# Optimization experiments

Hardware: AMD Instinct MI355X
Metric: run time of the kernel (lower is better)

## Reference

```python
import math
import jax, jax.numpy as jnp
import numpy as np

SR = 48000
FRAME_HOP = 240
F0_MIN = 20.0
F0_MAX = 5000.0
F0_BINS = 64
VEL_DIM = 8
N_HARM = 128
NOISE_FFT = 1024
N_NOISE = NOISE_FFT // 2 + 1
HOP = NOISE_FFT // 4
PAD = NOISE_FFT // 2


def lin_interp(x, size):
    # matches F.interpolate(mode='linear', align_corners=False) along last axis
    T_in = x.shape[-1]
    pos = (jnp.arange(size, dtype=jnp.float32) + 0.5) * (T_in / size) - 0.5
    pos = jnp.clip(pos, 0.0, T_in - 1.0)
    lo = jnp.floor(pos).astype(jnp.int32)
    hi = jnp.minimum(lo + 1, T_in - 1)
    fr = pos - lo.astype(jnp.float32)
    return x[..., lo] * (1.0 - fr) + x[..., hi] * fr


def encode_f0(f0):
    f0s = jnp.clip(f0, F0_MIN, None)
    fn = jnp.clip((jnp.log(f0s) - math.log(F0_MIN)) / (math.log(F0_MAX) - math.log(F0_MIN)), 0.0, 1.0)
    i = jnp.arange(1, F0_BINS // 2 + 1, dtype=jnp.float32)
    ang = math.pi * i * fn[..., None]  # (B,T,bins/2)
    enc = jnp.stack([jnp.sin(ang), jnp.cos(ang)], axis=-1).reshape(f0.shape + (F0_BINS,))
    return enc * (f0 > 0).astype(jnp.float32)[..., None]


def encode_velocity(vel):
    vn = jnp.clip(vel.astype(jnp.float32) / 7.0, 0.0, 1.0)
    i = jnp.arange(1, VEL_DIM // 2 + 1, dtype=jnp.float32)
    ang = math.pi * i * vn[..., None]
    return jnp.stack([jnp.sin(ang), jnp.cos(ang)], axis=-1).reshape(vel.shape + (VEL_DIM,))


def gru(x, W_ih, W_hh, b_ih, b_hh):
    # torch nn.GRU, 1 layer, batch_first; gate order r,z,n
    B, T, _ = x.shape
    H = W_hh.shape[1]
    gi = x @ W_ih.T + b_ih  # (B,T,3H)

    def step(h, g):
        gh = h @ W_hh.T + b_hh
        ir, iz, in_ = jnp.split(g, 3, axis=-1)
        hr, hz, hn = jnp.split(gh, 3, axis=-1)
        r = jax.nn.sigmoid(ir + hr)
        z = jax.nn.sigmoid(iz + hz)
        n = jnp.tanh(in_ + r * hn)
        h = (1.0 - z) * n + z * h
        return h, h

    _, hs = jax.lax.scan(step, jnp.zeros((B, H), x.dtype), jnp.swapaxes(gi, 0, 1))
    return jnp.swapaxes(hs, 0, 1)


def harmonic_synth(harm_amps, f0_hz, n_samples, inh):
    # harm_amps (B,T,N), f0_hz (B,T), inh (B,) -> (B,S)
    B, T, N = harm_amps.shape
    a = lin_interp(jnp.transpose(harm_amps, (0, 2, 1)), n_samples)        # (B,N,S)
    f0_up = lin_interp(f0_hz[:, None, :], n_samples)[:, 0]               # (B,S)
    k = jnp.arange(1, N + 1, dtype=jnp.float32)
    stretch = jnp.sqrt(1.0 + inh[:, None] * k ** 2)                      # (B,N)
    inst_freq = f0_up[:, None, :] * (k[None, :] * stretch)[:, :, None]   # (B,N,S)
    mask = (inst_freq < SR * 0.45).astype(a.dtype)
    f0_mean = f0_up.mean(axis=-1)
    n_active = jnp.maximum((k[None, :] * f0_mean[:, None] < SR * 0.45).sum(axis=1), 1).astype(a.dtype)
    phase = jnp.cumsum(2.0 * jnp.pi * inst_freq / SR, axis=-1)
    sig = (a * mask * jnp.sin(phase)).sum(axis=1)
    return sig / n_active[:, None]


def noise_synth(noise_mags, f0_hz, n_samples, noise):
    # noise_mags (B,T,513), noise (B,S) -> (B,S)
    B, T, N = noise_mags.shape
    window = 0.5 - 0.5 * jnp.cos(2.0 * jnp.pi * jnp.arange(NOISE_FFT, dtype=jnp.float32) / NOISE_FFT)  # hann, periodic
    padded = jnp.pad(noise, ((0, 0), (PAD, PAD)), mode='reflect')
    T_stft = 1 + n_samples // HOP
    idx = jnp.arange(T_stft)[:, None] * HOP + jnp.arange(NOISE_FFT)[None, :]  # (T_stft, n_fft)
    frames = padded[:, idx] * window                                          # (B,T_stft,n_fft)
    spec = jnp.fft.rfft(frames)                                               # (B,T_stft,513)
    mag_up = lin_interp(jnp.transpose(noise_mags, (0, 2, 1)), T_stft)         # (B,513,T_stft)
    f0_mean = jnp.clip(f0_hz, F0_MIN, None).mean(axis=1)                      # (B,)
    freqs = jnp.arange(N_NOISE, dtype=jnp.float32) * (SR / NOISE_FFT)
    src = jnp.clip(freqs[None, :] / f0_mean[:, None] * (N / N_HARM), 0.0, N - 1.0)  # (B,513)
    lo = src.astype(jnp.int32)
    hi = jnp.minimum(lo + 1, N - 1)
    fr = (src - lo.astype(jnp.float32))[:, :, None]
    lo_e = jnp.broadcast_to(lo[:, :, None], (B, N_NOISE, T_stft))
    hi_e = jnp.broadcast_to(hi[:, :, None], (B, N_NOISE, T_stft))
    v_lo = jnp.take_along_axis(mag_up, lo_e, axis=1)
    v_hi = jnp.take_along_axis(mag_up, hi_e, axis=1)
    mag_abs = v_lo + fr * (v_hi - v_lo)                                       # (B,513,T_stft)
    shaped = spec * jnp.transpose(mag_abs, (0, 2, 1))                         # (B,T_stft,513)
    tframes = jnp.fft.irfft(shaped, n=NOISE_FFT) * window                     # (B,T_stft,n_fft)
    Lp = NOISE_FFT + (T_stft - 1) * HOP
    flat = idx.reshape(-1)
    ola = jnp.zeros((B, Lp), jnp.float32).at[:, flat].add(tframes.reshape(B, -1))
    wsq = jnp.zeros((Lp,), jnp.float32).at[flat].add(jnp.tile(window ** 2, T_stft))
    out = ola / jnp.where(wsq > 1e-11, wsq, 1.0)
    return out[:, PAD:PAD + n_samples]


def ddsp_forward(f0_hz, loudness_db, noise_L, noise_R,
                 W_pre1, b_pre1, W_pre2, b_pre2, W_ih, W_hh, b_ih, b_hh,
                 W_post, b_post, W_harm, b_harm, W_amp, b_amp,
                 W_noise, b_noise, W_namp, b_namp, W_B, b_B, velocity):
    B, T = f0_hz.shape
    n_samples = T * FRAME_HOP
    feat = jnp.concatenate([encode_f0(f0_hz),
                            jnp.broadcast_to(encode_velocity(velocity)[:, None, :], (B, T, VEL_DIM))], axis=-1)
    feat = jax.nn.relu(feat @ W_pre1 + b_pre1)
    feat = jax.nn.relu(feat @ W_pre2 + b_pre2)
    feat = gru(feat, W_ih, W_hh, b_ih, b_hh)
    feat = jax.nn.relu(feat @ W_post + b_post)
    # stereo heads stacked on channel axis c in {L,R}
    harm_dist = jax.nn.softmax(jnp.einsum('btd,cdn->cbtn', feat, W_harm) + b_harm[:, None, None, :], axis=-1)
    harm_amp = jax.nn.softplus(jnp.einsum('btd,cd->cbt', feat, W_amp) + b_amp[:, None, None])
    harm_amps = harm_dist * harm_amp[..., None]                               # (2,B,T,128)
    nmag = jax.nn.sigmoid(jnp.einsum('btd,cdn->cbtn', feat, W_noise) + b_noise[:, None, None, :])
    nmag = nmag * jax.nn.softplus(jnp.einsum('btd,cd->cbt', feat, W_namp) + b_namp[:, None, None])[..., None]
    f0_mean = jnp.clip(f0_hz, F0_MIN, None).mean(axis=1)
    midi = 69.0 + 12.0 * jnp.log2(f0_mean / 440.0)
    b_max = 0.0008 * jnp.exp(-(midi - 21.0) / 88.0 * math.log(10.0))
    inh = jax.nn.sigmoid(feat @ W_B + b_B[0]).mean(axis=1) * b_max           # inh_scale = 1.0
    hL = harmonic_synth(harm_amps[0], f0_hz, n_samples, inh)
    hR = harmonic_synth(harm_amps[1], f0_hz, n_samples, inh)
    nL = noise_synth(nmag[0], f0_hz, n_samples, noise_L)
    nR = noise_synth(nmag[1], f0_hz, n_samples, noise_R)
    lo_up = lin_interp((10.0 ** (loudness_db / 20.0))[:, None, :], n_samples)[:, 0]
    return jnp.stack([(hL + nL) * lo_up, (hR + nR) * lo_up], axis=1)         # (B,2,S)


def setup_inputs() -> dict:
    key = jax.random.key(0)
    ks = iter(jax.random.split(key, 40))
    B, T = 2, 400
    S = T * FRAME_HOP
    rnd = lambda shape, s=0.05: jax.random.normal(next(ks), shape, jnp.float32) * s
    d = {}
    d['f0_hz'] = 100.0 + 400.0 * jax.random.uniform(next(ks), (B, T), jnp.float32)
    d['loudness_db'] = -30.0 + 5.0 * jax.random.normal(next(ks), (B, T), jnp.float32)
    d['noise_L'] = jax.random.normal(next(ks), (B, S), jnp.float32)
    d['noise_R'] = jax.random.normal(next(ks), (B, S), jnp.float32)
    d['W_pre1'] = rnd((72, 128)); d['b_pre1'] = rnd((128,))
    d['W_pre2'] = rnd((128, 128)); d['b_pre2'] = rnd((128,))
    d['W_ih'] = rnd((192, 128)); d['W_hh'] = rnd((192, 64))
    d['b_ih'] = rnd((192,)); d['b_hh'] = rnd((192,))
    d['W_post'] = rnd((64, 128)); d['b_post'] = rnd((128,))
    d['W_harm'] = rnd((2, 128, N_HARM)); d['b_harm'] = rnd((2, N_HARM))
    d['W_amp'] = rnd((2, 128)); d['b_amp'] = rnd((2,))
    d['W_noise'] = rnd((2, 128, N_NOISE)); d['b_noise'] = rnd((2, N_NOISE)) - 3.0
    d['W_namp'] = rnd((2, 128)); d['b_namp'] = rnd((2,)) - 3.0
    d['W_B'] = rnd((128,)); d['b_B'] = rnd((1,)) - 5.0
    d['velocity'] = jax.random.randint(next(ks), (B,), 0, 8, dtype=jnp.int32)
    return d


def reference(f0_hz, loudness_db, noise_L, noise_R,
              W_pre1, b_pre1, W_pre2, b_pre2, W_ih, W_hh, b_ih, b_hh,
              W_post, b_post, W_harm, b_harm, W_amp, b_amp,
              W_noise, b_noise, W_namp, b_namp, W_B, b_B, velocity):
    return ddsp_forward(f0_hz, loudness_db, noise_L, noise_R,
                        W_pre1, b_pre1, W_pre2, b_pre2, W_ih, W_hh, b_ih, b_hh,
                        W_post, b_post, W_harm, b_harm, W_amp, b_amp,
                        W_noise, b_noise, W_namp, b_namp, W_B, b_B, velocity)
```

## Files before the change

### kernel.cpp

```cpp
#include <hip/hip_runtime.h>
#include <math.h>

#define Tn   400
#define Bn   2
#define Sn   96000
#define NHh  128
#define NNn  513
#define NFFT 1024
#define HOPs 256
#define PADs 512
#define TS   376
#define LPn  97024
#define CUT  21600.0f
#define DPI  3.14159265358979323846

__device__ __forceinline__ float sigmoidf_(float x){ return 1.0f/(1.0f+expf(-x)); }
__device__ __forceinline__ float softplusf_(float x){ return fmaxf(x,0.0f)+log1pf(expf(-fabsf(x))); }
__device__ __forceinline__ float fsigmoid_(float x){ return __fdividef(1.0f, 1.0f + __expf(-x)); }
__device__ __forceinline__ float ftanh_(float x){
  float e = __expf(fminf(fmaxf(2.0f*x, -30.0f), 30.0f));
  return __fdividef(e - 1.0f, e + 1.0f);
}

__global__ void __launch_bounds__(128) k_frame1z(
    const float* f0, const int* vel,
    const float* Wp1, const float* bp1,
    const float* Wp2, const float* bp2,
    const float* Wih, const float* bih,
    float* gi, float4* olaz, float* fs, double* P) {
  int blk = blockIdx.x;
  int tid = threadIdx.x;
  if (blk >= Bn*Tn) {
    if (blk == Bn*Tn) {
      int b = tid;
      if (b < Bn) {
        const float* f = f0 + b*Tn;
        double sm = 0.0;
        for (int t=0;t<Tn;t++) sm += fmax((double)f[t], 20.0);
        float f0m = (float)(sm / (double)Tn);
        fs[b] = f0m;
        float midi = 69.0f + 12.0f * log2f(f0m/440.0f);
        fs[2+b] = 0.0008f * expf(-(midi-21.0f)*(1.0f/88.0f) * 2.302585093f);
        double* Pb = P + b*Tn;
        double acc = 0.0;
        for (int m=0;m<Tn;m++){ Pb[m] = acc; if (m < Tn-1) acc += (double)f[m] + (double)f[m+1]; }
        double Ctot = 120.0*((double)f[0] + Pb[Tn-1] + (double)f[Tn-1]);
        double fupmean = Ctot / (double)Sn;
        int cnt = 0;
        for (int k=1;k<=NHh;k++) if ((float)k * (float)fupmean < CUT) cnt++;
        if (cnt < 1) cnt = 1;
        fs[4+b] = (float)cnt;
        fs[6+b] = 0.0f;
      }
    } else {
      int base = (blk - (Bn*Tn+1))*512 + tid;
      #pragma unroll
      for (int r=0;r<4;r++) {
        int idx = base + r*128;
        if (idx < 97024) olaz[idx] = make_float4(0.f,0.f,0.f,0.f);
      }
    }
    return;
  }
  int b = blk / Tn, t = blk % Tn;
  __shared__ float x[72];
  __shared__ float y1[128];
  __shared__ float y2[128];
  if (tid < 72) {
    if (tid < 64) {
      float fv = f0[b*Tn+t];
      float fsv = fmaxf(fv, 20.0f);
      float fn = (logf(fsv) - 2.99573227355399f) * (1.0f/5.52146091786225f);
      fn = fminf(fmaxf(fn,0.0f),1.0f);
      int j = (tid>>1) + 1;
      float ang = (float)DPI * (float)j * fn;
      x[tid] = (tid & 1) ? cosf(ang) : sinf(ang);
    } else {
      int i = tid - 64;
      float vn = fminf(fmaxf((float)vel[b]*(1.0f/7.0f),0.0f),1.0f);
      int j = (i>>1)+1;
      float ang = (float)DPI * (float)j * vn;
      x[tid] = (i & 1) ? cosf(ang) : sinf(ang);
    }
  }
  __syncthreads();
  {
    float a = bp1[tid];
    #pragma unroll 8
    for (int i=0;i<72;i++) a += x[i]*Wp1[i*128+tid];
    y1[tid] = fmaxf(a,0.0f);
  }
  __syncthreads();
  {
    float a = bp2[tid];
    #pragma unroll 8
    for (int i=0;i<128;i++) a += y1[i]*Wp2[i*128+tid];
    y2[tid] = fmaxf(a,0.0f);
  }
  __syncthreads();
  float* gout = gi + ((size_t)b*Tn + t)*192;
  for (int g = tid; g < 192; g += 128) {
    float s = bih[g];
    const float* wr = Wih + g*128;
    #pragma unroll 8
    for (int d=0; d<128; d++) s += y2[d]*wr[d];
    gout[g] = s;
  }
}

__global__ void __launch_bounds__(832, 1) k_grufft(
    const float* __restrict__ gi, const float* __restrict__ Whh,
    const float* __restrict__ bhh, float* __restrict__ hsout,
    const float* __restrict__ noiseL, const float* __restrict__ noiseR,
    float2* __restrict__ spec) {
  __shared__ float h[64];
  __shared__ float sp[768];
  __shared__ float re[1024], im[1024];
  __shared__ float twc[512], tws[512];
  __shared__ float wdw[1024];
  int j = threadIdx.x;

  if (blockIdx.x >= 2) {
    if (j >= 256) return;
    int idx = blockIdx.x - 2;
    int sig = idx / TS, t = idx % TS;
    int b = sig >> 1, c = sig & 1;
    const float* noise = (c==0 ? noiseL : noiseR) + (size_t)b*Sn;
    int tid = j;
    for (int q=tid; q<512; q+=256) {
      float ang = (float)(2.0*DPI) * (float)q * (1.0f/1024.0f);
      twc[q] = cosf(ang); tws[q] = sinf(ang);
    }
    for (int i=tid; i<1024; i+=256)
      wdw[i] = 0.5f - 0.5f*cosf((float)(2.0*DPI)*(float)i*(1.0f/1024.0f));
    __syncthreads();
    for (int i=tid;i<1024;i+=256) {
      int q = t*HOPs + i - PADs;
      if (q < 0) q = -q;
      if (q >= Sn) q = 2*Sn - 2 - q;
      float v = noise[q]*wdw[i];
      int br = (int)(__brev((unsigned)i) >> 22);
      re[br] = v; im[br] = 0.0f;
    }
    __syncthreads();
    for (int st=1; st<=10; st++) {
      int half = 1<<(st-1);
      #pragma unroll
      for (int w=0;w<2;w++) {
        int bid = tid + w*256;
        int pos = bid & (half-1);
        int i0 = ((bid >> (st-1)) << st) + pos;
        int i1 = i0 + half;
        int q = pos << (10-st);
        float cr = twc[q], ci = -tws[q];
        float xr = re[i1], xi = im[i1];
        float tr = cr*xr - ci*xi, ti = cr*xi + ci*xr;
        float ar = re[i0], ai = im[i0];
        re[i1] = ar - tr; im[i1] = ai - ti;
        re[i0] = ar + tr; im[i0] = ai + ti;
      }
      __syncthreads();
    }
    float2* so = spec + ((size_t)sig*TS + t)*NNn;
    for (int k=tid;k<=512;k+=256) so[k] = make_float2(re[k], im[k]);
    return;
  }

  int b = blockIdx.x;
  const float* gib = gi + (size_t)b*Tn*192;
  float* hb_ = hsout + (size_t)b*Tn*64;
  int wv = j >> 6, lane = j & 63;
  int p = wv / 3;
  int row = (wv % 3)*64 + lane;
  float4 w0,w1,w2,w3;
  if (j < 768) {
    const float4* W4 = (const float4*)(Whh + (size_t)row*64 + p*16);
    w0=W4[0]; w1=W4[1]; w2=W4[2]; w3=W4[3];
    if (j < 64) h[j] = 0.0f;
  }
  int u = lane;
  float hu = 0.0f, br=0.f, bz=0.f, bn=0.f;
  float ga[8], gz_[8], gn_[8], hist[8];
  if (j >= 768) {
    br = bhh[u]; bz = bhh[64+u]; bn = bhh[128+u];
    #pragma unroll
    for (int i=0;i<8;i++) {
      ga[i]  = gib[(size_t)i*192 + u];
      gz_[i] = gib[(size_t)i*192 + 64 + u];
      gn_[i] = gib[(size_t)i*192 + 128 + u];
    }
  }
  __syncthreads();

  for (int c=0;c<50;c++) {
    #pragma unroll
    for (int i=0;i<8;i++) {
      if (j < 768) {
        const float4* h4 = (const float4*)h;
        float4 x0=h4[p*4+0], x1=h4[p*4+1], x2=h4[p*4+2], x3=h4[p*4+3];
        float a0,a1,a2,a3;
        a0 = w0.x*x0.x; a1 = w0.y*x0.y; a2 = w0.z*x0.z; a3 = w0.w*x0.w;
        a0 = fmaf(w1.x,x1.x,a0); a1 = fmaf(w1.y,x1.y,a1);
        a2 = fmaf(w1.z,x1.z,a2); a3 = fmaf(w1.w,x1.w,a3);
        a0 = fmaf(w2.x,x2.x,a0); a1 = fmaf(w2.y,x2.y,a1);
        a2 = fmaf(w2.z,x2.z,a2); a3 = fmaf(w2.w,x2.w,a3);
        a0 = fmaf(w3.x,x3.x,a0); a1 = fmaf(w3.y,x3.y,a1);
        a2 = fmaf(w3.z,x3.z,a2); a3 = fmaf(w3.w,x3.w,a3);
        sp[p*192 + row] = (a0+a1)+(a2+a3);
      }
      __syncthreads();
      if (j >= 768) {
        float mr = (sp[u]      + sp[192+u])     + (sp[384+u]     + sp[576+u]);
        float mz = (sp[64+u]   + sp[192+64+u])  + (sp[384+64+u]  + sp[576+64+u]);
        float mn = (sp[128+u]  + sp[192+128+u]) + (sp[384+128+u] + sp[576+128+u]);
        float rg = fsigmoid_(ga[i]  + br + mr);
        float zg = fsigmoid_(gz_[i] + bz + mz);
        float ng = ftanh_(gn_[i] + rg*(bn + mn));
        hu = (1.0f - zg)*ng + zg*hu;
        h[u] = hu;
        hist[i] = hu;
      }
      __syncthreads();
    }
    if (j >= 768) {
      int t0 = c*8;
      #pragma unroll
      for (int i=0;i<8;i++) hb_[(size_t)(t0+i)*64 + u] = hist[i];
      if (c < 49) {
        int t1 = t0 + 8;
        #pragma unroll
        for (int i=0;i<8;i++) {
          ga[i]  = gib[(size_t)(t1+i)*192 + u];
          gz_[i] = gib[(size_t)(t1+i)*192 + 64 + u];
          gn_[i] = gib[(size_t)(t1+i)*192 + 128 + u];
        }
      }
    }
  }
}

__global__ void __launch_bounds__(256) k_heads(
    const float* hs, const float* Wpost, const float* bpost,
    const float* Wharm, const float* bharm,
    const float* Wamp, const float* bamp,
    const float* Wnoise, const float* bnoise,
    const float* Wnamp, const float* bnamp,
    const float* WB, const float* bB,
    float* harm, float* nmag, float* fs) {
  int bt = blockIdx.x; int b = bt / Tn, t = bt % Tn;
  __shared__ float h64[64];
  __shared__ float fp[128];
  __shared__ float lg[256];
  __shared__ float red[8];
  int tid = threadIdx.x;
  if (tid < 64) h64[tid] = hs[((size_t)b*Tn+t)*64+tid];
  __syncthreads();
  if (tid < 128) {
    float a = bpost[tid];
    #pragma unroll 8
    for (int i=0;i<64;i++) a += h64[i]*Wpost[i*128+tid];
    fp[tid] = fmaxf(a,0.0f);
  }
  __syncthreads();
  {
    int c = tid >> 7, n = tid & 127;
    float a = bharm[c*128+n];
    const float* w = Wharm + (size_t)c*128*128 + n;
    #pragma unroll 8
    for (int d=0;d<128;d++) a += fp[d]*w[d*128];
    lg[tid] = a;
  }
  __syncthreads();
  if (tid < 2) {
    const float* l = lg + tid*128;
    float mx = l[0];
    for (int n=1;n<128;n++) mx = fmaxf(mx,l[n]);
    float sm = 0.f; for (int n=0;n<128;n++) sm += expf(l[n]-mx);
    red[tid] = mx; red[2+tid] = sm;
    float aa = bamp[tid];
    for (int d=0;d<128;d++) aa += fp[d]*Wamp[tid*128+d];
    red[4+tid] = softplusf_(aa);
    float na = bnamp[tid];
    for (int d=0;d<128;d++) na += fp[d]*Wnamp[tid*128+d];
    red[6+tid] = softplusf_(na);
  } else if (tid == 2) {
    float bb = bB[0];
    for (int d=0;d<128;d++) bb += fp[d]*WB[d];
    atomicAdd(&fs[6+b], sigmoidf_(bb));
  }
  __syncthreads();
  {
    int c = tid >> 7, n = tid & 127;
    float v = expf(lg[tid]-red[c]) / red[2+c] * red[4+c];
    harm[(((size_t)c*Bn + b)*Tn + t)*128 + n] = v;
  }
  for (int o = tid; o < 2*NNn; o += 256) {
    int c = (o < NNn) ? 0 : 1; int n = o - c*NNn;
    float a = bnoise[c*NNn+n];
    const float* w = Wnoise + (size_t)c*128*NNn + n;
    #pragma unroll 8
    for (int d=0;d<128;d++) a += fp[d]*w[(size_t)d*NNn];
    nmag[(((size_t)c*Bn + b)*Tn + t)*NNn + n] = sigmoidf_(a) * red[6+c];
  }
}

__global__ void __launch_bounds__(256) k_harmnoise(
    const float* __restrict__ f0, const float* __restrict__ harm,
    const double* __restrict__ P, const float* __restrict__ fs,
    float* __restrict__ sigh,
    const float2* __restrict__ spec, const float* __restrict__ nmag,
    float* __restrict__ ola) {
  __shared__ double rks[128];
  __shared__ float  rkf[128];
  __shared__ float re[1024], im[1024];
  __shared__ float twc[512], tws[512];
  __shared__ float wdw[1024];
  int tid = threadIdx.x;

  if (blockIdx.x < 750) {
    int b = blockIdx.x / 375;
    int s = (blockIdx.x % 375)*256 + tid;
    if (tid < 128) {
      float inhf = fs[6+b]*(1.0f/(float)Tn) * fs[2+b];
      double inh = (double)inhf;
      double kk = (double)(tid+1);
      double r = kk * sqrt(1.0 + inh*kk*kk);
      rks[tid] = r; rkf[tid] = (float)r;
    }
    __syncthreads();
    const float* f = f0 + b*Tn;
    float posf = ((float)s + 0.5f) * (400.0f/96000.0f) - 0.5f;
    posf = fminf(fmaxf(posf, 0.0f), 399.0f);
    int lo = (int)floorf(posf);
    int hi = min(lo+1, 399);
    float fr = posf - (float)lo;
    float f0up = f[lo]*(1.0f-fr) + f[hi]*fr;
    double C;
    if (s < 120) {
      C = (double)(s+1) * (double)f[0];
    } else if (s < 95880) {
      int m = (s-120)/240;
      int q = s - 120 - 240*m;
      double fm = (double)f[m], fm1 = (double)f[m+1];
      double jp = (double)(q+1);
      C = 120.0*((double)f[0] + P[b*Tn+m]) + jp*fm + (fm1-fm)*jp*jp*(1.0/480.0);
    } else {
      C = 120.0*((double)f[0] + P[b*Tn+399]) + (double)(s-95880+1)*(double)f[399];
    }
    double Phi = C * (2.0*DPI/48000.0);
    const float* hLlo = harm + (((size_t)0*Bn + b)*Tn + lo)*128;
    const float* hLhi = harm + (((size_t)0*Bn + b)*Tn + hi)*128;
    const float* hRlo = harm + (((size_t)1*Bn + b)*Tn + lo)*128;
    const float* hRhi = harm + (((size_t)1*Bn + b)*Tn + hi)*128;
    float accL=0.f, accR=0.f;
    for (int k=0;k<128;k++) {
      float finst = f0up * rkf[k];
      if (finst < CUT) {
        double u = rks[k]*Phi * (1.0/(2.0*DPI));
        u -= floor(u);
        float sv = __sinf((float)u * 6.28318530717959f);
        float aL = hLlo[k]*(1.0f-fr) + hLhi[k]*fr;
        float aR = hRlo[k]*(1.0f-fr) + hRhi[k]*fr;
        accL += aL*sv; accR += aR*sv;
      }
    }
    float na = fs[4+b];
    sigh[((size_t)b*2+0)*Sn + s] = accL/na;
    sigh[((size_t)b*2+1)*Sn + s] = accR/na;
    return;
  }

  int idx = blockIdx.x - 750;
  int sig = idx / TS, t = idx % TS;
  int b = sig >> 1, c = sig & 1;
  for (int q=tid; q<512; q+=256) {
    float ang = (float)(2.0*DPI) * (float)q * (1.0f/1024.0f);
    twc[q] = cosf(ang); tws[q] = sinf(ang);
  }
  for (int i=tid; i<1024; i+=256)
    wdw[i] = 0.5f - 0.5f*cosf((float)(2.0*DPI)*(float)i*(1.0f/1024.0f));
  float f0m = fs[b];
  float pp = ((float)t + 0.5f) * (400.0f/376.0f) - 0.5f;
  pp = fminf(fmaxf(pp,0.0f),399.0f);
  int tlo = (int)floorf(pp); int thi = min(tlo+1, 399); float tfr = pp - (float)tlo;
  const float* nm = nmag + (((size_t)c*Bn + b)*Tn)*NNn;
  const float2* so = spec + ((size_t)sig*TS + t)*NNn;
  for (int k=tid;k<=512;k+=256) {
    float src = (float)k * 46.875f / f0m * (513.0f/128.0f);
    src = fminf(fmaxf(src,0.0f),512.0f);
    int flo = (int)src; int fhi = min(flo+1,512); float ffr = src - (float)flo;
    float vlo = nm[(size_t)tlo*NNn+flo]*(1.0f-tfr) + nm[(size_t)thi*NNn+flo]*tfr;
    float vhi = nm[(size_t)tlo*NNn+fhi]*(1.0f-tfr) + nm[(size_t)thi*NNn+fhi]*tfr;
    float mag = vlo + ffr*(vhi-vlo);
    float2 v = so[k];
    re[k] = v.x*mag; im[k] = v.y*mag;
  }
  __syncthreads();
  for (int k=tid+513; k<1024; k+=256) {
    re[k] = re[1024-k]; im[k] = -im[1024-k];
  }
  __syncthreads();
  for (int i=tid;i<1024;i+=256) {
    int jx = (int)(__brev((unsigned)i)>>22);
    if (i < jx) {
      float a=re[i]; re[i]=re[jx]; re[jx]=a;
      float bb=im[i]; im[i]=im[jx]; im[jx]=bb;
    }
  }
  __syncthreads();
  for (int st=1; st<=10; st++) {
    int half = 1<<(st-1);
    #pragma unroll
    for (int w=0;w<2;w++) {
      int bid = tid + w*256;
      int pos = bid & (half-1);
      int i0 = ((bid >> (st-1)) << st) + pos;
      int i1 = i0 + half;
      int q = pos << (10-st);
      float cr = twc[q], ci = tws[q];
      float xr = re[i1], xi = im[i1];
      float tr = cr*xr - ci*xi, ti = cr*xi + ci*xr;
      float ar = re[i0], ai = im[i0];
      re[i1] = ar - tr; im[i1] = ai - ti;
      re[i0] = ar + tr; im[i0] = ai + ti;
    }
    __syncthreads();
  }
  float* olab = ola + (size_t)sig*LPn;
  for (int i=tid;i<1024;i+=256) {
    float y = re[i] * (1.0f/1024.0f) * wdw[i];
    atomicAdd(&olab[t*HOPs + i], y);
  }
}

__global__ void __launch_bounds__(256) k_final(
    const float* loud, const float* sigh, const float* ola, float* out) {
  int b = blockIdx.y;
  int s = blockIdx.x*256 + threadIdx.x;
  float posf = ((float)s + 0.5f)*(400.0f/96000.0f) - 0.5f;
  posf = fminf(fmaxf(posf,0.0f),399.0f);
  int lo=(int)floorf(posf); int hi=min(lo+1,399); float fr=posf-(float)lo;
  const float* ld = loud + b*Tn;
  float lv = exp10f(ld[lo]*0.05f)*(1.0f-fr) + exp10f(ld[hi]*0.05f)*fr;
  int p = PADs + s;
  float wsq;
  if (s >= 511 && s <= 95743) {
    wsq = 1.5f;
  } else {
    int t0 = (p >= 1023) ? ((p - 1023 + 255) >> 8) : 0;
    int t1 = min(TS-1, p >> 8);
    wsq = 0.0f;
    for (int t=t0;t<=t1;t++) {
      int i = p - (t<<8);
      float w = 0.5f - 0.5f*cosf((float)(2.0*DPI)*(float)i*(1.0f/1024.0f));
      wsq += w*w;
    }
  }
  float denom = (wsq > 1e-11f) ? wsq : 1.0f;
  for (int c=0;c<2;c++) {
    float hv = sigh[((size_t)b*2+c)*Sn+s];
    float nv = ola[(size_t)(b*2+c)*LPn + p] / denom;
    out[((size_t)b*2+c)*Sn + s] = (hv + nv)*lv;
  }
}

extern "C" void kernel_launch(void* const* d_in, const int* in_sizes, int n_in,
                              void* d_out, int out_size, void* d_ws, size_t ws_size,
                              hipStream_t stream) {
  const float* f0    = (const float*)d_in[0];
  const float* loud  = (const float*)d_in[1];
  const float* nL    = (const float*)d_in[2];
  const float* nR    = (const float*)d_in[3];
  const float* Wp1   = (const float*)d_in[4];  const float* bp1 = (const float*)d_in[5];
  const float* Wp2   = (const float*)d_in[6];  const float* bp2 = (const float*)d_in[7];
  const float* Wih   = (const float*)d_in[8];  const float* Whh = (const float*)d_in[9];
  const float* bih   = (const float*)d_in[10]; const float* bhh = (const float*)d_in[11];
  const float* Wpost = (const float*)d_in[12]; const float* bpost=(const float*)d_in[13];
  const float* Wharm = (const float*)d_in[14]; const float* bharm=(const float*)d_in[15];
  const float* Wamp  = (const float*)d_in[16]; const float* bamp =(const float*)d_in[17];
  const float* Wnoise= (const float*)d_in[18]; const float* bnoise=(const float*)d_in[19];
  const float* Wnamp = (const float*)d_in[20]; const float* bnamp=(const float*)d_in[21];
  const float* WB    = (const float*)d_in[22]; const float* bB  = (const float*)d_in[23];
  const int*   vel   = (const int*)d_in[24];
  float* out = (float*)d_out;

  char* w = (char*)d_ws;
  double* P    = (double*)w; w += (size_t)Bn*Tn*sizeof(double);
  double* rk   = (double*)w; w += (size_t)Bn*128*sizeof(double);
  float* gi    = (float*)w;  w += (size_t)Bn*Tn*192*sizeof(float);
  float* hsb   = (float*)w;  w += (size_t)Bn*Tn*64*sizeof(float);
  float* harm  = (float*)w;  w += (size_t)2*Bn*Tn*128*sizeof(float);
  float* nmag  = (float*)w;  w += (size_t)2*Bn*Tn*NNn*sizeof(float);
  float* sigh  = (float*)w;  w += (size_t)Bn*2*Sn*sizeof(float);
  float* ola   = (float*)w;  w += (size_t)Bn*2*LPn*sizeof(float);
  float* fscal = (float*)w;  w += 32*sizeof(float);
  float2* spec = (float2*)w; w += (size_t)4*TS*NNn*sizeof(float2);
  (void)rk;

  int nzblk = (97024 + 511) / 512;
  k_frame1z<<<Bn*Tn + 1 + nzblk, 128, 0, stream>>>(
      f0, vel, Wp1,bp1, Wp2,bp2, Wih,bih, gi, (float4*)ola, fscal, P);
  k_grufft<<<2 + 4*TS, 832, 0, stream>>>(gi, Whh, bhh, hsb, nL, nR, spec);
  k_heads<<<Bn*Tn, 256, 0, stream>>>(hsb, Wpost,bpost, Wharm,bharm, Wamp,bamp,
                                     Wnoise,bnoise, Wnamp,bnamp, WB,bB,
                                     harm, nmag, fscal);
  k_harmnoise<<<750 + 4*TS, 256, 0, stream>>>(f0, harm, P, fscal, sigh,
                                              spec, nmag, ola);
  dim3 gf(Sn/256, Bn);
  k_final<<<gf, 256, 0, stream>>>(loud, sigh, ola, out);
}
```

Measured before the change: 391.5 us.

## Shrink GRU recurrence block to 448 threads with 2-way K split

Reworks the GRU recurrence partitioning so that each thread computes half of the 64-length dot product (32 weights in registers) instead of a quarter. This drops from 12 to 6 matvec waves plus one gate wave, halves the shared partial-sum buffer and the reduction adds. The gate-input prefetch chunk also grows from 8 to 16 timesteps. The goal is fewer waves contending at each barrier and cheaper per-step reductions, in exchange for longer per-thread FMA chains and more registers. The FFT blocks now launch with 448 threads and still use only 256, so fewer threads sit idle.

```diff
diff --git a/kernel.cpp b/kernel.cpp
--- a/kernel.cpp
+++ b/kernel.cpp
@@ -108,13 +108,13 @@
   }
 }
 
-__global__ void __launch_bounds__(832, 1) k_grufft(
+__global__ void __launch_bounds__(448, 1) k_grufft(
     const float* __restrict__ gi, const float* __restrict__ Whh,
     const float* __restrict__ bhh, float* __restrict__ hsout,
     const float* __restrict__ noiseL, const float* __restrict__ noiseR,
     float2* __restrict__ spec) {
   __shared__ float h[64];
-  __shared__ float sp[768];
+  __shared__ float sp[384];
   __shared__ float re[1024], im[1024];
   __shared__ float twc[512], tws[512];
   __shared__ float wdw[1024];
@@ -170,34 +170,35 @@
   const float* gib = gi + (size_t)b*Tn*192;
   float* hb_ = hsout + (size_t)b*Tn*64;
   int wv = j >> 6, lane = j & 63;
-  int p = wv / 3;
-  int row = (wv % 3)*64 + lane;
-  float4 w0,w1,w2,w3;
-  if (j < 768) {
-    const float4* W4 = (const float4*)(Whh + (size_t)row*64 + p*16);
+  int p = wv & 1;
+  int row = (wv >> 1)*64 + lane;
+  float4 w0,w1,w2,w3,w4,w5,w6,w7;
+  if (wv < 6) {
+    const float4* W4 = (const float4*)(Whh + (size_t)row*64 + p*32);
     w0=W4[0]; w1=W4[1]; w2=W4[2]; w3=W4[3];
+    w4=W4[4]; w5=W4[5]; w6=W4[6]; w7=W4[7];
     if (j < 64) h[j] = 0.0f;
   }
-  int u = lane;
   float hu = 0.0f, br=0.f, bz=0.f, bn=0.f;
-  float ga[8], gz_[8], gn_[8], hist[8];
-  if (j >= 768) {
-    br = bhh[u]; bz = bhh[64+u]; bn = bhh[128+u];
+  float ga[16], gz_[16], gn_[16], hist[16];
+  if (wv == 6) {
+    br = bhh[lane]; bz = bhh[64+lane]; bn = bhh[128+lane];
     #pragma unroll
-    for (int i=0;i<8;i++) {
-      ga[i]  = gib[(size_t)i*192 + u];
-      gz_[i] = gib[(size_t)i*192 + 64 + u];
-      gn_[i] = gib[(size_t)i*192 + 128 + u];
-    }
-  }
-  __syncthreads();
-
-  for (int c=0;c<50;c++) {
+    for (int i=0;i<16;i++) {
+      ga[i]  = gib[(size_t)i*192 + lane];
+      gz_[i] = gib[(size_t)i*192 + 64 + lane];
+      gn_[i] = gib[(size_t)i*192 + 128 + lane];
+    }
+  }
+  __syncthreads();
+
+  for (int c=0;c<25;c++) {
     #pragma unroll
-    for (int i=0;i<8;i++) {
-      if (j < 768) {
+    for (int i=0;i<16;i++) {
+      if (wv < 6) {
         const float4* h4 = (const float4*)h;
-        float4 x0=h4[p*4+0], x1=h4[p*4+1], x2=h4[p*4+2], x3=h4[p*4+3];
+        float4 x0=h4[p*8+0], x1=h4[p*8+1], x2=h4[p*8+2], x3=h4[p*8+3];
+        float4 x4=h4[p*8+4], x5=h4[p*8+5], x6=h4[p*8+6], x7=h4[p*8+7];
         float a0,a1,a2,a3;
         a0 = w0.x*x0.x; a1 = w0.y*x0.y; a2 = w0.z*x0.z; a3 = w0.w*x0.w;
         a0 = fmaf(w1.x,x1.x,a0); a1 = fmaf(w1.y,x1.y,a1);
@@ -206,33 +207,41 @@
         a2 = fmaf(w2.z,x2.z,a2); a3 = fmaf(w2.w,x2.w,a3);
         a0 = fmaf(w3.x,x3.x,a0); a1 = fmaf(w3.y,x3.y,a1);
         a2 = fmaf(w3.z,x3.z,a2); a3 = fmaf(w3.w,x3.w,a3);
+        a0 = fmaf(w4.x,x4.x,a0); a1 = fmaf(w4.y,x4.y,a1);
+        a2 = fmaf(w4.z,x4.z,a2); a3 = fmaf(w4.w,x4.w,a3);
+        a0 = fmaf(w5.x,x5.x,a0); a1 = fmaf(w5.y,x5.y,a1);
+        a2 = fmaf(w5.z,x5.z,a2); a3 = fmaf(w5.w,x5.w,a3);
+        a0 = fmaf(w6.x,x6.x,a0); a1 = fmaf(w6.y,x6.y,a1);
+        a2 = fmaf(w6.z,x6.z,a2); a3 = fmaf(w6.w,x6.w,a3);
+        a0 = fmaf(w7.x,x7.x,a0); a1 = fmaf(w7.y,x7.y,a1);
+        a2 = fmaf(w7.z,x7.z,a2); a3 = fmaf(w7.w,x7.w,a3);
         sp[p*192 + row] = (a0+a1)+(a2+a3);
       }
       __syncthreads();
-      if (j >= 768) {
-        float mr = (sp[u]      + sp[192+u])     + (sp[384+u]     + sp[576+u]);
-        float mz = (sp[64+u]   + sp[192+64+u])  + (sp[384+64+u]  + sp[576+64+u]);
-        float mn = (sp[128+u]  + sp[192+128+u]) + (sp[384+128+u] + sp[576+128+u]);
+      if (wv == 6) {
+        float mr = sp[lane]     + sp[192+lane];
+        float mz = sp[64+lane]  + sp[256+lane];
+        float mn = sp[128+lane] + sp[320+lane];
         float rg = fsigmoid_(ga[i]  + br + mr);
         float zg = fsigmoid_(gz_[i] + bz + mz);
         float ng = ftanh_(gn_[i] + rg*(bn + mn));
         hu = (1.0f - zg)*ng + zg*hu;
-        h[u] = hu;
+        h[lane] = hu;
         hist[i] = hu;
       }
       __syncthreads();
     }
-    if (j >= 768) {
-      int t0 = c*8;
+    if (wv == 6) {
+      int t0 = c*16;
       #pragma unroll
-      for (int i=0;i<8;i++) hb_[(size_t)(t0+i)*64 + u] = hist[i];
-      if (c < 49) {
-        int t1 = t0 + 8;
+      for (int i=0;i<16;i++) hb_[(size_t)(t0+i)*64 + lane] = hist[i];
+      if (c < 24) {
+        int t1 = t0 + 16;
         #pragma unroll
-        for (int i=0;i<8;i++) {
-          ga[i]  = gib[(size_t)(t1+i)*192 + u];
-          gz_[i] = gib[(size_t)(t1+i)*192 + 64 + u];
-          gn_[i] = gib[(size_t)(t1+i)*192 + 128 + u];
+        for (int i=0;i<16;i++) {
+          ga[i]  = gib[(size_t)(t1+i)*192 + lane];
+          gz_[i] = gib[(size_t)(t1+i)*192 + 64 + lane];
+          gn_[i] = gib[(size_t)(t1+i)*192 + 128 + lane];
         }
       }
     }
@@ -500,7 +509,7 @@
   int nzblk = (97024 + 511) / 512;
   k_frame1z<<<Bn*Tn + 1 + nzblk, 128, 0, stream>>>(
       f0, vel, Wp1,bp1, Wp2,bp2, Wih,bih, gi, (float4*)ola, fscal, P);
-  k_grufft<<<2 + 4*TS, 832, 0, stream>>>(gi, Whh, bhh, hsb, nL, nR, spec);
+  k_grufft<<<2 + 4*TS, 448, 0, stream>>>(gi, Whh, bhh, hsb, nL, nR, spec);
   k_heads<<<Bn*Tn, 256, 0, stream>>>(hsb, Wpost,bpost, Wharm,bharm, Wamp,bamp,
                                      Wnoise,bnoise, Wnamp,bnamp, WB,bB,
                                      harm, nmag, fscal);
```

After: 398.9 us. No clear change (+1.9%).
